# Performance work log

Measured on AMD Instinct MI355X. Metric: run time of the kernel, lower is better.

Reference implementation:

```python
import jax, jax.numpy as jnp
import numpy as np

NEG_BIG = -9e15  # matches torch's -9000000000000000.0 mask value


def _gat_layer(x, adj_mask, W, a):
    # x: [N, Fin], W: [Fin, Fout], a: [Fout]
    h = x @ W                                   # [N, Fout]
    d = jnp.abs(h[None, :, :] - h[:, None, :])  # [N, N, Fout] pairwise |h_j - h_i|
    e = jax.nn.relu(jnp.einsum('ijf,f->ij', d, a))
    e = jnp.where(adj_mask, e, NEG_BIG)
    att = jax.nn.softmax(e, axis=1)             # row softmax (dropout p=0, skipped)
    return jax.nn.relu(att @ h)


def setup_inputs() -> dict:
    key = jax.random.key(0)
    ks = jax.random.split(key, 10)
    N, F, H, C = 1024, 128, 128, 16

    def xavier(k, shape, gain=1.414):
        fan_in, fan_out = shape[0], shape[-1]
        bound = gain * np.sqrt(6.0 / (fan_in + fan_out))
        return jax.random.uniform(k, shape, jnp.float32, -bound, bound)

    feat = jax.random.normal(ks[0], (N, F), jnp.float32)
    adj = jax.random.randint(ks[1], (N, N), 0, 2, jnp.int32)
    return {
        'feat': feat,
        'adj': adj,
        'W1': xavier(ks[2], (F, H)), 'a1': xavier(ks[3], (H, 1)).squeeze(-1),
        'W2': xavier(ks[4], (H, H)), 'a2': xavier(ks[5], (H, 1)).squeeze(-1),
        'W3': xavier(ks[6], (H, H)), 'a3': xavier(ks[7], (H, 1)).squeeze(-1),
        'Wfc': xavier(ks[8], (H, C), gain=1.0),
        'bfc': jnp.zeros((C,), jnp.float32),
    }


def reference(feat, adj, W1, a1, W2, a2, W3, a3, Wfc, bfc):
    mask = adj > 0
    x = _gat_layer(feat, mask, W1, a1)
    x = _gat_layer(x, mask, W2, a2)
    x = _gat_layer(x, mask, W3, a3)
    # EdgeGCN (include_adj=False): pairwise abs-diff -> linear, output [N*N, C]
    N, H = x.shape
    diff = jnp.abs(x[None, :, :] - x[:, None, :]).reshape(N * N, H)
    return diff @ Wfc + bfc
```

## Files before the change

kernel.cpp:

```cpp
#include <hip/hip_runtime.h>
#include <math.h>

#define NEG_BIG -9.0e15f

typedef __attribute__((ext_vector_type(4))) float f32x4;
typedef __attribute__((ext_vector_type(8))) short bf16x8;
typedef __attribute__((ext_vector_type(4))) unsigned int u32x4;

__global__ __launch_bounds__(128) void gemm_xw_t(const float* __restrict__ X,
                                                 const float* __restrict__ W,
                                                 float* __restrict__ HT) {
  __shared__ float xrow[128];
  const int i = blockIdx.x;
  const int o = threadIdx.x;
  xrow[o] = X[(size_t)i * 128 + o];
  __syncthreads();
  float acc = 0.f;
#pragma unroll 16
  for (int k = 0; k < 128; ++k) acc = fmaf(xrow[k], W[(size_t)k * 128 + o], acc);
  HT[(size_t)o * 1024 + i] = acc;
}

#define DOT4(acc, hv, p) \
  acc = fmaf(hv.x, p.x, fmaf(hv.y, p.y, fmaf(hv.z, p.z, fmaf(hv.w, p.w, acc))));

#define ABSFMA4R(accR, hv, hs, av)                  \
  accR.x = fmaf(fabsf(hv.x - hs), av, accR.x);      \
  accR.y = fmaf(fabsf(hv.y - hs), av, accR.y);      \
  accR.z = fmaf(fabsf(hv.z - hs), av, accR.z);      \
  accR.w = fmaf(fabsf(hv.w - hs), av, accR.w);

__global__ __launch_bounds__(1024, 4) void gat_attn(const float* __restrict__ HT,
                                                    const int* __restrict__ adj,
                                                    const float* __restrict__ a,
                                                    float* __restrict__ Xout) {
  __shared__ float4 ep4[4][4][256];
  __shared__ float e_s[4][1024];
  __shared__ float4 h4_s[128];
  __shared__ float a_s[128];
  __shared__ float redm[4][4];
  __shared__ float redsum[4][4];
  __shared__ float inv_s[4];

  const int t = threadIdx.x;
  const int i0 = blockIdx.x * 4;
  const float4* __restrict__ HT4 = reinterpret_cast<const float4*>(HT);

  if (t < 128) {
    h4_s[t] = *reinterpret_cast<const float4*>(HT + ((size_t)t << 10) + i0);
    a_s[t] = a[t];
  }
  __syncthreads();

  const int fq = t >> 8;
  const int jt = t & 255;
  const int il = t >> 8;
  const int j0 = jt * 4;

  float4 ac0 = {0.f, 0.f, 0.f, 0.f};
  float4 ac1 = {0.f, 0.f, 0.f, 0.f};
  float4 ac2 = {0.f, 0.f, 0.f, 0.f};
  float4 ac3 = {0.f, 0.f, 0.f, 0.f};
#pragma unroll 8
  for (int ff = 0; ff < 32; ++ff) {
    const int f = fq * 32 + ff;
    const float4 hv = HT4[f * 256 + jt];
    const float4 h4 = h4_s[f];
    const float av = a_s[f];
    ABSFMA4R(ac0, hv, h4.x, av);
    ABSFMA4R(ac1, hv, h4.y, av);
    ABSFMA4R(ac2, hv, h4.z, av);
    ABSFMA4R(ac3, hv, h4.w, av);
  }
  ep4[fq][0][jt] = ac0;
  ep4[fq][1][jt] = ac1;
  ep4[fq][2][jt] = ac2;
  ep4[fq][3][jt] = ac3;
  __syncthreads();

  float4 esum;
  {
    const float4 s0 = ep4[0][il][jt];
    const float4 s1 = ep4[1][il][jt];
    const float4 s2 = ep4[2][il][jt];
    const float4 s3 = ep4[3][il][jt];
    esum.x = (s0.x + s1.x) + (s2.x + s3.x);
    esum.y = (s0.y + s1.y) + (s2.y + s3.y);
    esum.z = (s0.z + s1.z) + (s2.z + s3.z);
    esum.w = (s0.w + s1.w) + (s2.w + s3.w);
  }

  float4 e;
  {
    const int4 ad = *reinterpret_cast<const int4*>(&adj[(size_t)(i0 + il) * 1024 + j0]);
    e.x = ad.x > 0 ? fmaxf(esum.x, 0.f) : NEG_BIG;
    e.y = ad.y > 0 ? fmaxf(esum.y, 0.f) : NEG_BIG;
    e.z = ad.z > 0 ? fmaxf(esum.z, 0.f) : NEG_BIG;
    e.w = ad.w > 0 ? fmaxf(esum.w, 0.f) : NEG_BIG;
  }

  const int wq = (t >> 6) & 3;
  float m = fmaxf(fmaxf(e.x, e.y), fmaxf(e.z, e.w));
#pragma unroll
  for (int off = 32; off > 0; off >>= 1) m = fmaxf(m, __shfl_xor(m, off));
  if ((t & 63) == 0) redm[il][wq] = m;
  __syncthreads();
  m = fmaxf(fmaxf(redm[il][0], redm[il][1]), fmaxf(redm[il][2], redm[il][3]));
  float4 p;
  p.x = __expf(e.x - m);
  p.y = __expf(e.y - m);
  p.z = __expf(e.z - m);
  p.w = __expf(e.w - m);
  *reinterpret_cast<float4*>(&e_s[il][j0]) = p;
  float s = p.x + p.y + p.z + p.w;
#pragma unroll
  for (int off = 32; off > 0; off >>= 1) s += __shfl_xor(s, off);
  if ((t & 63) == 0) redsum[il][wq] = s;
  __syncthreads();
  if (t < 4) {
    const float ss = redsum[t][0] + redsum[t][1] + redsum[t][2] + redsum[t][3];
    inv_s[t] = 1.f / ss;
  }
  __syncthreads();

  const int w = t >> 6;
  const int l = t & 63;
  const int f0 = w * 8;
  float acc[8][4];
#pragma unroll
  for (int ff = 0; ff < 8; ++ff)
#pragma unroll
    for (int r = 0; r < 4; ++r) acc[ff][r] = 0.f;

#pragma unroll
  for (int jb = 0; jb < 4; ++jb) {
    const int j4 = jb * 64 + l;
    const float4 p0 = *reinterpret_cast<const float4*>(&e_s[0][j4 * 4]);
    const float4 p1 = *reinterpret_cast<const float4*>(&e_s[1][j4 * 4]);
    const float4 p2 = *reinterpret_cast<const float4*>(&e_s[2][j4 * 4]);
    const float4 p3 = *reinterpret_cast<const float4*>(&e_s[3][j4 * 4]);
#pragma unroll
    for (int ff = 0; ff < 8; ++ff) {
      const float4 hv = HT4[(f0 + ff) * 256 + j4];
      DOT4(acc[ff][0], hv, p0);
      DOT4(acc[ff][1], hv, p1);
      DOT4(acc[ff][2], hv, p2);
      DOT4(acc[ff][3], hv, p3);
    }
  }

  float v[32];
#pragma unroll
  for (int ff = 0; ff < 8; ++ff)
#pragma unroll
    for (int r = 0; r < 4; ++r) v[ff * 4 + r] = acc[ff][r];

#pragma unroll
  for (int step = 0; step < 5; ++step) {
    const int s2 = 1 << step;
    const bool hi = (l & s2) != 0;
#pragma unroll
    for (int k = 0; k < (32 >> (step + 1)); ++k) {
      const float x = v[2 * k];
      const float y = v[2 * k + 1];
      float tt = hi ? x : y;
      tt = __shfl_xor(tt, s2);
      v[k] = (hi ? y : x) + tt;
    }
  }
  float r = v[0] + __shfl_xor(v[0], 32);

  if (l < 32) {
    const int oidx = l & 31;
    const int ff = oidx >> 2;
    const int orow = oidx & 3;
    const float o = fmaxf(r * inv_s[orow], 0.f);
    Xout[(size_t)(i0 + orow) * 128 + f0 + ff] = o;
  }
}

__global__ __launch_bounds__(256) void edge_fc_mfma(const float* __restrict__ X,
                                                    const float* __restrict__ Wfc,
                                                    const float* __restrict__ bfc,
                                                    float* __restrict__ out) {
  __shared__ float xi_s[32][132];
  __shared__ float xj_s[32][132];
  __shared__ float ostage[4][256];

  const int t = threadIdx.x;
  const int ib = blockIdx.x >> 5;
  const int jb = blockIdx.x & 31;

  {
    const int r = t >> 3;
    const int c0 = (t & 7) * 16;
    const float4* gi = reinterpret_cast<const float4*>(X + (size_t)(ib * 32 + r) * 128 + c0);
    const float4* gj = reinterpret_cast<const float4*>(X + (size_t)(jb * 32 + r) * 128 + c0);
#pragma unroll
    for (int k = 0; k < 4; ++k) {
      *reinterpret_cast<float4*>(&xi_s[r][c0 + k * 4]) = gi[k];
      *reinterpret_cast<float4*>(&xj_s[r][c0 + k * 4]) = gj[k];
    }
  }

  const int w = t >> 6, lane = t & 63;
  const int col = lane & 15, kg = lane >> 4;

  bf16x8 bhi[4], blo[4];
#pragma unroll
  for (int c = 0; c < 4; ++c) {
    bf16x8 bh, bl;
#pragma unroll
    for (int j = 0; j < 8; ++j) {
      const float wv = Wfc[(c * 32 + kg * 8 + j) * 16 + col];
      const unsigned u = __builtin_bit_cast(unsigned, wv);
      const unsigned h = u & 0xffff0000u;
      const float lof = wv - __builtin_bit_cast(float, h);
      bh[j] = (short)(h >> 16);
      bl[j] = (short)(__builtin_bit_cast(unsigned, lof) >> 16);
    }
    bhi[c] = bh;
    blo[c] = bl;
  }
  const float bb = bfc[col];

  __syncthreads();

  const int j0 = (w & 1) * 16;
  const int ih = w >> 1;
  unsigned xjr[4][8];
#pragma unroll
  for (int c = 0; c < 4; ++c) {
    const float4 v0 = *reinterpret_cast<const float4*>(&xj_s[j0 + col][c * 32 + kg * 8]);
    const float4 v1 = *reinterpret_cast<const float4*>(&xj_s[j0 + col][c * 32 + kg * 8 + 4]);
    xjr[c][0] = __builtin_bit_cast(unsigned, v0.x);
    xjr[c][1] = __builtin_bit_cast(unsigned, v0.y);
    xjr[c][2] = __builtin_bit_cast(unsigned, v0.z);
    xjr[c][3] = __builtin_bit_cast(unsigned, v0.w);
    xjr[c][4] = __builtin_bit_cast(unsigned, v1.x);
    xjr[c][5] = __builtin_bit_cast(unsigned, v1.y);
    xjr[c][6] = __builtin_bit_cast(unsigned, v1.z);
    xjr[c][7] = __builtin_bit_cast(unsigned, v1.w);
  }

  for (int i = 0; i < 16; ++i) {
    const int li = ih * 16 + i;
    const int gi = ib * 32 + li;
    f32x4 acc = {bb, bb, bb, bb};
#pragma unroll
    for (int c = 0; c < 4; ++c) {
      const float4 v0 = *reinterpret_cast<const float4*>(&xi_s[li][c * 32 + kg * 8]);
      const float4 v1 = *reinterpret_cast<const float4*>(&xi_s[li][c * 32 + kg * 8 + 4]);
      unsigned xiv[8];
      xiv[0] = __builtin_bit_cast(unsigned, v0.x);
      xiv[1] = __builtin_bit_cast(unsigned, v0.y);
      xiv[2] = __builtin_bit_cast(unsigned, v0.z);
      xiv[3] = __builtin_bit_cast(unsigned, v0.w);
      xiv[4] = __builtin_bit_cast(unsigned, v1.x);
      xiv[5] = __builtin_bit_cast(unsigned, v1.y);
      xiv[6] = __builtin_bit_cast(unsigned, v1.z);
      xiv[7] = __builtin_bit_cast(unsigned, v1.w);
      u32x4 ahv, alv;
#pragma unroll
      for (int q = 0; q < 4; ++q) {
        const float d0 = __builtin_bit_cast(float, xjr[c][2 * q]) -
                         __builtin_bit_cast(float, xiv[2 * q]);
        const float d1 = __builtin_bit_cast(float, xjr[c][2 * q + 1]) -
                         __builtin_bit_cast(float, xiv[2 * q + 1]);
        const unsigned h0 = __builtin_bit_cast(unsigned, d0) & 0x7fff0000u;
        const unsigned h1 = __builtin_bit_cast(unsigned, d1) & 0x7fff0000u;
        const float lo0 = fabsf(d0) - __builtin_bit_cast(float, h0);
        const float lo1 = fabsf(d1) - __builtin_bit_cast(float, h1);
        ahv[q] = __builtin_amdgcn_perm(h1, h0, 0x07060302u);
        alv[q] = __builtin_amdgcn_perm(__builtin_bit_cast(unsigned, lo1),
                                       __builtin_bit_cast(unsigned, lo0), 0x07060302u);
      }
      const bf16x8 ah = __builtin_bit_cast(bf16x8, ahv);
      const bf16x8 al = __builtin_bit_cast(bf16x8, alv);
      acc = __builtin_amdgcn_mfma_f32_16x16x32_bf16(ah, bhi[c], acc, 0, 0, 0);
      acc = __builtin_amdgcn_mfma_f32_16x16x32_bf16(ah, blo[c], acc, 0, 0, 0);
      acc = __builtin_amdgcn_mfma_f32_16x16x32_bf16(al, bhi[c], acc, 0, 0, 0);
    }
#pragma unroll
    for (int r = 0; r < 4; ++r) ostage[w][(kg * 4 + r) * 16 + col] = acc[r];
    const f32x4 vv = *reinterpret_cast<const f32x4*>(&ostage[w][lane * 4]);
    const int jl = lane >> 2;
    const int c0 = (lane & 3) * 4;
    const int gj = jb * 32 + j0 + jl;
    __builtin_nontemporal_store(vv, reinterpret_cast<f32x4*>(out + ((size_t)gi * 1024 + gj) * 16 + c0));
  }
}

extern "C" void kernel_launch(void* const* d_in, const int* in_sizes, int n_in,
                              void* d_out, int out_size, void* d_ws, size_t ws_size,
                              hipStream_t stream) {
  const float* feat = (const float*)d_in[0];
  const int* adj = (const int*)d_in[1];
  const float* W1 = (const float*)d_in[2];
  const float* a1 = (const float*)d_in[3];
  const float* W2 = (const float*)d_in[4];
  const float* a2 = (const float*)d_in[5];
  const float* W3 = (const float*)d_in[6];
  const float* a3 = (const float*)d_in[7];
  const float* Wfc = (const float*)d_in[8];
  const float* bfc = (const float*)d_in[9];
  float* out = (float*)d_out;

  float* ht = (float*)d_ws;
  float* xA = ht + 131072;
  float* xB = xA + 131072;

  gemm_xw_t<<<1024, 128, 0, stream>>>(feat, W1, ht);
  gat_attn<<<256, 1024, 0, stream>>>(ht, adj, a1, xA);
  gemm_xw_t<<<1024, 128, 0, stream>>>(xA, W2, ht);
  gat_attn<<<256, 1024, 0, stream>>>(ht, adj, a2, xB);
  gemm_xw_t<<<1024, 128, 0, stream>>>(xB, W3, ht);
  gat_attn<<<256, 1024, 0, stream>>>(ht, adj, a3, xA);
  edge_fc_mfma<<<1024, 256, 0, stream>>>(xA, Wfc, bfc, out);
}
```

Measured before the change: 102.1 us.

## Give each wave both j-tiles and store MFMA results directly without LDS staging

In the edge FC kernel, each wave now keeps both 16-column j halves in registers and processes 8 i rows, running two MFMA accumulator chains per row instead of one. This reuses each loaded xi row across both j tiles and gives the scheduler two independent MFMA chains to interleave. The output is written straight from the accumulators with scalar nontemporal stores, removing the LDS staging buffer and its write-then-read round trip. The costs are more registers per thread and 4-byte stores in place of 16-byte vector stores, which may be less efficient for the large output write.

Result: no change. 102.4 us (+0.3%).

```diff
diff --git a/kernel.cpp b/kernel.cpp
--- a/kernel.cpp
+++ b/kernel.cpp
@@ -185,7 +185,6 @@
                                                     float* __restrict__ out) {
   __shared__ float xi_s[32][132];
   __shared__ float xj_s[32][132];
-  __shared__ float ostage[4][256];
 
   const int t = threadIdx.x;
   const int ib = blockIdx.x >> 5;
@@ -226,27 +225,31 @@
 
   __syncthreads();
 
-  const int j0 = (w & 1) * 16;
-  const int ih = w >> 1;
-  unsigned xjr[4][8];
-#pragma unroll
-  for (int c = 0; c < 4; ++c) {
-    const float4 v0 = *reinterpret_cast<const float4*>(&xj_s[j0 + col][c * 32 + kg * 8]);
-    const float4 v1 = *reinterpret_cast<const float4*>(&xj_s[j0 + col][c * 32 + kg * 8 + 4]);
-    xjr[c][0] = __builtin_bit_cast(unsigned, v0.x);
-    xjr[c][1] = __builtin_bit_cast(unsigned, v0.y);
-    xjr[c][2] = __builtin_bit_cast(unsigned, v0.z);
-    xjr[c][3] = __builtin_bit_cast(unsigned, v0.w);
-    xjr[c][4] = __builtin_bit_cast(unsigned, v1.x);
-    xjr[c][5] = __builtin_bit_cast(unsigned, v1.y);
-    xjr[c][6] = __builtin_bit_cast(unsigned, v1.z);
-    xjr[c][7] = __builtin_bit_cast(unsigned, v1.w);
-  }
-
-  for (int i = 0; i < 16; ++i) {
-    const int li = ih * 16 + i;
+  unsigned xjr[2][4][8];
+#pragma unroll
+  for (int jt = 0; jt < 2; ++jt) {
+#pragma unroll
+    for (int c = 0; c < 4; ++c) {
+      const float4 v0 = *reinterpret_cast<const float4*>(&xj_s[jt * 16 + col][c * 32 + kg * 8]);
+      const float4 v1 = *reinterpret_cast<const float4*>(&xj_s[jt * 16 + col][c * 32 + kg * 8 + 4]);
+      xjr[jt][c][0] = __builtin_bit_cast(unsigned, v0.x);
+      xjr[jt][c][1] = __builtin_bit_cast(unsigned, v0.y);
+      xjr[jt][c][2] = __builtin_bit_cast(unsigned, v0.z);
+      xjr[jt][c][3] = __builtin_bit_cast(unsigned, v0.w);
+      xjr[jt][c][4] = __builtin_bit_cast(unsigned, v1.x);
+      xjr[jt][c][5] = __builtin_bit_cast(unsigned, v1.y);
+      xjr[jt][c][6] = __builtin_bit_cast(unsigned, v1.z);
+      xjr[jt][c][7] = __builtin_bit_cast(unsigned, v1.w);
+    }
+  }
+
+  const int iq = w;
+
+  for (int i = 0; i < 8; ++i) {
+    const int li = iq * 8 + i;
     const int gi = ib * 32 + li;
-    f32x4 acc = {bb, bb, bb, bb};
+    f32x4 acc0 = {bb, bb, bb, bb};
+    f32x4 acc1 = {bb, bb, bb, bb};
 #pragma unroll
     for (int c = 0; c < 4; ++c) {
       const float4 v0 = *reinterpret_cast<const float4*>(&xi_s[li][c * 32 + kg * 8]);
@@ -260,34 +263,44 @@
       xiv[5] = __builtin_bit_cast(unsigned, v1.y);
       xiv[6] = __builtin_bit_cast(unsigned, v1.z);
       xiv[7] = __builtin_bit_cast(unsigned, v1.w);
-      u32x4 ahv, alv;
-#pragma unroll
-      for (int q = 0; q < 4; ++q) {
-        const float d0 = __builtin_bit_cast(float, xjr[c][2 * q]) -
-                         __builtin_bit_cast(float, xiv[2 * q]);
-        const float d1 = __builtin_bit_cast(float, xjr[c][2 * q + 1]) -
-                         __builtin_bit_cast(float, xiv[2 * q + 1]);
-        const unsigned h0 = __builtin_bit_cast(unsigned, d0) & 0x7fff0000u;
-        const unsigned h1 = __builtin_bit_cast(unsigned, d1) & 0x7fff0000u;
-        const float lo0 = fabsf(d0) - __builtin_bit_cast(float, h0);
-        const float lo1 = fabsf(d1) - __builtin_bit_cast(float, h1);
-        ahv[q] = __builtin_amdgcn_perm(h1, h0, 0x07060302u);
-        alv[q] = __builtin_amdgcn_perm(__builtin_bit_cast(unsigned, lo1),
-                                       __builtin_bit_cast(unsigned, lo0), 0x07060302u);
+#pragma unroll
+      for (int jt = 0; jt < 2; ++jt) {
+        u32x4 ahv, alv;
+#pragma unroll
+        for (int q = 0; q < 4; ++q) {
+          const float d0 = __builtin_bit_cast(float, xjr[jt][c][2 * q]) -
+                           __builtin_bit_cast(float, xiv[2 * q]);
+          const float d1 = __builtin_bit_cast(float, xjr[jt][c][2 * q + 1]) -
+                           __builtin_bit_cast(float, xiv[2 * q + 1]);
+          const unsigned h0 = __builtin_bit_cast(unsigned, d0) & 0x7fff0000u;
+          const unsigned h1 = __builtin_bit_cast(unsigned, d1) & 0x7fff0000u;
+          const float lo0 = fabsf(d0) - __builtin_bit_cast(float, h0);
+          const float lo1 = fabsf(d1) - __builtin_bit_cast(float, h1);
+          ahv[q] = __builtin_amdgcn_perm(h1, h0, 0x07060302u);
+          alv[q] = __builtin_amdgcn_perm(__builtin_bit_cast(unsigned, lo1),
+                                         __builtin_bit_cast(unsigned, lo0), 0x07060302u);
+        }
+        const bf16x8 ah = __builtin_bit_cast(bf16x8, ahv);
+        const bf16x8 al = __builtin_bit_cast(bf16x8, alv);
+        if (jt == 0) {
+          acc0 = __builtin_amdgcn_mfma_f32_16x16x32_bf16(ah, bhi[c], acc0, 0, 0, 0);
+          acc0 = __builtin_amdgcn_mfma_f32_16x16x32_bf16(ah, blo[c], acc0, 0, 0, 0);
+          acc0 = __builtin_amdgcn_mfma_f32_16x16x32_bf16(al, bhi[c], acc0, 0, 0, 0);
+        } else {
+          acc1 = __builtin_amdgcn_mfma_f32_16x16x32_bf16(ah, bhi[c], acc1, 0, 0, 0);
+          acc1 = __builtin_amdgcn_mfma_f32_16x16x32_bf16(ah, blo[c], acc1, 0, 0, 0);
+          acc1 = __builtin_amdgcn_mfma_f32_16x16x32_bf16(al, bhi[c], acc1, 0, 0, 0);
+        }
       }
-      const bf16x8 ah = __builtin_bit_cast(bf16x8, ahv);
-      const bf16x8 al = __builtin_bit_cast(bf16x8, alv);
-      acc = __builtin_amdgcn_mfma_f32_16x16x32_bf16(ah, bhi[c], acc, 0, 0, 0);
-      acc = __builtin_amdgcn_mfma_f32_16x16x32_bf16(ah, blo[c], acc, 0, 0, 0);
-      acc = __builtin_amdgcn_mfma_f32_16x16x32_bf16(al, bhi[c], acc, 0, 0, 0);
-    }
-#pragma unroll
-    for (int r = 0; r < 4; ++r) ostage[w][(kg * 4 + r) * 16 + col] = acc[r];
-    const f32x4 vv = *reinterpret_cast<const f32x4*>(&ostage[w][lane * 4]);
-    const int jl = lane >> 2;
-    const int c0 = (lane & 3) * 4;
-    const int gj = jb * 32 + j0 + jl;
-    __builtin_nontemporal_store(vv, reinterpret_cast<f32x4*>(out + ((size_t)gi * 1024 + gj) * 16 + c0));
+    }
+    const size_t obase = (size_t)gi * 1024;
+#pragma unroll
+    for (int r = 0; r < 4; ++r) {
+      const int gj0 = jb * 32 + kg * 4 + r;
+      const int gj1 = gj0 + 16;
+      __builtin_nontemporal_store(acc0[r], out + (obase + gj0) * 16 + col);
+      __builtin_nontemporal_store(acc1[r], out + (obase + gj1) * 16 + col);
+    }
   }
 }
 
```
